# Kernel tuning notes

Measured on AMD Instinct MI355X. Metric: run time of the kernel, lower is better.

## Reference

```python
import jax, jax.numpy as jnp
import numpy as np

B, C, H, W = 4, 512, 48, 48
DQ = C // 8  # inter_rate = 8
N = H * W
EPS = 1e-5


def _local_mask(radius):
    r = np.arange(N) // W
    c = np.arange(N) % W
    d = np.maximum(np.abs(r[:, None] - r[None, :]), np.abs(c[:, None] - c[None, :]))
    return jnp.asarray(d <= radius)


def setup_inputs() -> dict:
    key = jax.random.key(0)
    ks = jax.random.split(key, 12)
    def nrm(k, shape, scale=0.04):
        return jax.random.normal(k, shape, dtype=jnp.float32) * scale
    zc = jnp.zeros((C,), jnp.float32)
    oc = jnp.ones((C,), jnp.float32)
    return {
        "x": jax.random.normal(ks[0], (B, C, H, W), dtype=jnp.float32),
        "Wq": nrm(ks[1], (DQ, C)), "bq": jnp.zeros((DQ,), jnp.float32),
        "Wk": nrm(ks[2], (DQ, C)), "bk": jnp.zeros((DQ,), jnp.float32),
        "Wv": nrm(ks[3], (C, C)), "bv": zc,
        "conv1_w": nrm(ks[4], (C, C, 3, 3)),
        "bn1_w": oc, "bn1_b": zc, "bn1_m": zc, "bn1_v": oc,
        "conv2_w": nrm(ks[5], (C, C, 3, 3)),
        "bn2_w": oc, "bn2_b": zc, "bn2_m": zc, "bn2_v": oc,
        "sig1_w": nrm(ks[6], (C, C)), "sig1_b": zc,
        "sig2_w": nrm(ks[7], (C, C)), "sig2_b": zc,
        "gamma": jnp.full((1,), 0.5, jnp.float32),
        "gamma1": jnp.full((1,), 0.3, jnp.float32),
        "gamma2": jnp.full((1,), 0.2, jnp.float32),
        "mask1": _local_mask(6),
        "mask2": _local_mask(12),
    }


def _masked_softmax(e, mask):
    # exp(e)*mask / sum(exp(e)*mask) == softmax with -inf outside mask
    e = e - jnp.max(e, axis=-1, keepdims=True)
    w = jnp.exp(e) * mask.astype(e.dtype)
    return w / jnp.sum(w, axis=-1, keepdims=True)


def _conv1x1(t, w, b):
    return jnp.einsum('bchw,dc->bdhw', t, w) + b[None, :, None, None]


def _conv3x3_bn_relu(t, w, g, beta, mu, var):
    y = jax.lax.conv_general_dilated(t, w, (1, 1), 'SAME',
                                     dimension_numbers=('NCHW', 'OIHW', 'NCHW'))
    scale = (g / jnp.sqrt(var + EPS))[None, :, None, None]
    y = (y - mu[None, :, None, None]) * scale + beta[None, :, None, None]
    return jax.nn.relu(y)


def _forward(x, Wq, bq, Wk, bk, Wv, bv, conv1_w, bn1_w, bn1_b, bn1_m, bn1_v,
             conv2_w, bn2_w, bn2_b, bn2_m, bn2_v, sig1_w, sig1_b, sig2_w, sig2_b,
             gamma, gamma1, gamma2, mask1, mask2):
    b, c, h, w = x.shape
    n = h * w
    q = _conv1x1(x, Wq, bq).reshape(b, -1, n)   # [B, d, N]
    k = _conv1x1(x, Wk, bk).reshape(b, -1, n)   # [B, d, N]
    energy = jnp.einsum('bdn,bdm->bnm', q, k)   # [B, N, N] (query rows)
    a0 = jax.nn.softmax(energy, axis=-1)
    a1 = _masked_softmax(energy, mask1)
    a2 = _masked_softmax(energy, mask2)
    v = _conv1x1(x, Wv, bv).reshape(b, c, n)
    # torch: bmm(value, attention.permute(0,2,1)) -> out[b,c,m] = sum_n v[b,c,n]*a[m,n]
    out0 = jnp.einsum('bcn,bmn->bcm', v, a0).reshape(b, c, h, w)
    out0 = gamma * out0 + x
    out0 = _conv3x3_bn_relu(out0, conv1_w, bn1_w, bn1_b, bn1_m, bn1_v)
    s1 = (jax.nn.sigmoid(_conv1x1(out0, sig1_w, sig1_b)) * out0).reshape(b, c, n)
    out1 = jnp.einsum('bcn,bmn->bcm', s1, a1).reshape(b, c, h, w)
    out1 = gamma1 * out1 + out0
    out1 = _conv3x3_bn_relu(out1, conv2_w, bn2_w, bn2_b, bn2_m, bn2_v)
    s2 = (jax.nn.sigmoid(_conv1x1(out1, sig2_w, sig2_b)) * out1).reshape(b, c, n)
    out2 = jnp.einsum('bcn,bmn->bcm', s2, a2).reshape(b, c, h, w)
    return gamma2 * out2 + out1


def reference(x, Wq, bq, Wk, bk, Wv, bv, conv1_w, bn1_w, bn1_b, bn1_m, bn1_v,
              conv2_w, bn2_w, bn2_b, bn2_m, bn2_v, sig1_w, sig1_b, sig2_w, sig2_b,
              gamma, gamma1, gamma2, mask1, mask2):
    return _forward(x, Wq, bq, Wk, bk, Wv, bv, conv1_w, bn1_w, bn1_b, bn1_m, bn1_v,
                    conv2_w, bn2_w, bn2_b, bn2_m, bn2_v, sig1_w, sig1_b, sig2_w, sig2_b,
                    gamma, gamma1, gamma2, mask1, mask2)
```

## Files before the change

### kernel.cpp

```cpp
#include <hip/hip_runtime.h>
#include <math.h>

#define BB 4
#define CC 512
#define HH 48
#define WW 48
#define NN 2304
#define DDQ 64
#define LDSP 72
#define PW 50
#define PROWS 2500

typedef __attribute__((ext_vector_type(4))) float f32x4;
typedef __attribute__((ext_vector_type(8))) _Float16 half8;
typedef __attribute__((ext_vector_type(4))) _Float16 half4;
typedef __attribute__((ext_vector_type(8))) short bf16x8;

__device__ __forceinline__ int imax(int a, int b) { return a > b ? a : b; }
__device__ __forceinline__ int imin(int a, int b) { return a < b ? a : b; }
__device__ __forceinline__ int prow(int m) {
    int h = m / WW, w = m - h * WW;
    return (h + 1) * PW + (w + 1);
}
__device__ __forceinline__ unsigned short f2bf(float f) {
    unsigned u = __float_as_uint(f);
    u += 0x7fffu + ((u >> 16) & 1u);
    return (unsigned short)(u >> 16);
}
__device__ __forceinline__ float bf2f(unsigned short s) {
    unsigned u = ((unsigned)s) << 16;
    return __uint_as_float(u);
}

typedef __attribute__((address_space(1))) unsigned int g_u32;
typedef __attribute__((address_space(3))) unsigned int l_u32;
__device__ __forceinline__ void gl16(const void* g, void* l) {
    __builtin_amdgcn_global_load_lds((const g_u32*)g, (l_u32*)l, 16, 0, 0);
}

#define WAIT6()  asm volatile("s_waitcnt vmcnt(6)" ::: "memory")
#define WAIT0()  asm volatile("s_waitcnt vmcnt(0)" ::: "memory")
#define BAR()    { __builtin_amdgcn_s_barrier(); asm volatile("" ::: "memory"); }

#define BWAVE_IDX()                                  \
    int tid = threadIdx.x;                           \
    int wave = tid >> 6, lane = tid & 63;            \
    int wm = (wave >> 1) * 64, wn = (wave & 1) * 32; \
    int x = lane & 15, qq = lane >> 4;

__device__ __forceinline__ half8 fragld(const _Float16* T, int r, int c) {
    int kb = c ^ (r & 7);
    return *(const half8*)(T + r * 64 + kb * 8);
}
__device__ __forceinline__ bf16x8 fragld_b(const unsigned short* T, int r, int c) {
    int kb = c ^ (r & 7);
    return *(const bf16x8*)(T + r * 64 + kb * 8);
}

__device__ __forceinline__ void btile(const _Float16* As, const _Float16* Bs,
                                      f32x4 acc[4][2], int wm, int wn, int x, int qq) {
#pragma unroll
    for (int ks = 0; ks < 2; ++ks) {
        int c = ks * 4 + qq;
        half8 a0 = fragld(As, wm + x, c);
        half8 a1 = fragld(As, wm + 16 + x, c);
        half8 a2 = fragld(As, wm + 32 + x, c);
        half8 a3 = fragld(As, wm + 48 + x, c);
        half8 b0 = fragld(Bs, wn + x, c);
        half8 b1 = fragld(Bs, wn + 16 + x, c);
        acc[0][0] = __builtin_amdgcn_mfma_f32_16x16x32_f16(a0, b0, acc[0][0], 0, 0, 0);
        acc[0][1] = __builtin_amdgcn_mfma_f32_16x16x32_f16(a0, b1, acc[0][1], 0, 0, 0);
        acc[1][0] = __builtin_amdgcn_mfma_f32_16x16x32_f16(a1, b0, acc[1][0], 0, 0, 0);
        acc[1][1] = __builtin_amdgcn_mfma_f32_16x16x32_f16(a1, b1, acc[1][1], 0, 0, 0);
        acc[2][0] = __builtin_amdgcn_mfma_f32_16x16x32_f16(a2, b0, acc[2][0], 0, 0, 0);
        acc[2][1] = __builtin_amdgcn_mfma_f32_16x16x32_f16(a2, b1, acc[2][1], 0, 0, 0);
        acc[3][0] = __builtin_amdgcn_mfma_f32_16x16x32_f16(a3, b0, acc[3][0], 0, 0, 0);
        acc[3][1] = __builtin_amdgcn_mfma_f32_16x16x32_f16(a3, b1, acc[3][1], 0, 0, 0);
    }
}
__device__ __forceinline__ void btile_b(const unsigned short* As, const unsigned short* Bs,
                                        f32x4 acc[4][2], int wm, int wn, int x, int qq) {
#pragma unroll
    for (int ks = 0; ks < 2; ++ks) {
        int c = ks * 4 + qq;
        bf16x8 a0 = fragld_b(As, wm + x, c);
        bf16x8 a1 = fragld_b(As, wm + 16 + x, c);
        bf16x8 a2 = fragld_b(As, wm + 32 + x, c);
        bf16x8 a3 = fragld_b(As, wm + 48 + x, c);
        bf16x8 b0 = fragld_b(Bs, wn + x, c);
        bf16x8 b1 = fragld_b(Bs, wn + 16 + x, c);
        acc[0][0] = __builtin_amdgcn_mfma_f32_16x16x32_bf16(a0, b0, acc[0][0], 0, 0, 0);
        acc[0][1] = __builtin_amdgcn_mfma_f32_16x16x32_bf16(a0, b1, acc[0][1], 0, 0, 0);
        acc[1][0] = __builtin_amdgcn_mfma_f32_16x16x32_bf16(a1, b0, acc[1][0], 0, 0, 0);
        acc[1][1] = __builtin_amdgcn_mfma_f32_16x16x32_bf16(a1, b1, acc[1][1], 0, 0, 0);
        acc[2][0] = __builtin_amdgcn_mfma_f32_16x16x32_bf16(a2, b0, acc[2][0], 0, 0, 0);
        acc[2][1] = __builtin_amdgcn_mfma_f32_16x16x32_bf16(a2, b1, acc[2][1], 0, 0, 0);
        acc[3][0] = __builtin_amdgcn_mfma_f32_16x16x32_bf16(a3, b0, acc[3][0], 0, 0, 0);
        acc[3][1] = __builtin_amdgcn_mfma_f32_16x16x32_bf16(a3, b1, acc[3][1], 0, 0, 0);
    }
}

#define BACC_INIT()                                         \
    f32x4 zf = {0.f, 0.f, 0.f, 0.f};                        \
    f32x4 acc[4][2];                                        \
    _Pragma("unroll") for (int i_ = 0; i_ < 4; ++i_) {      \
        acc[i_][0] = zf; acc[i_][1] = zf; }

#define SLOT_A(i) int sb = (wave * 4 + (i)) * 64; int s = sb + lane; \
                  int r = s >> 3, kb = s & 7; int koff = ((kb ^ (r & 7)) << 3);
#define SLOT_B(i) int sb = (wave * 2 + (i)) * 64; int s = sb + lane; \
                  int r = s >> 3, kb = s & 7; int koff = ((kb ^ (r & 7)) << 3);

__device__ __forceinline__ void stage_rows(_Float16* dst, const _Float16* __restrict__ src,
                                           int ld, int row0, int k0, int tid) {
#pragma unroll
    for (int i = 0; i < 2; ++i) {
        int s = tid * 2 + i;
        int r = s >> 3, off = (s & 7) << 3;
        *(half8*)(dst + r * LDSP + off) =
            *(const half8*)(src + (size_t)(row0 + r) * ld + k0 + off);
    }
}
__device__ __forceinline__ void mfma_tile(const _Float16* As, const _Float16* Bs,
                                          f32x4 acc[2][2], int wm, int wn, int x, int qq) {
#pragma unroll
    for (int ks = 0; ks < 2; ++ks) {
        int kof = ks * 32 + qq * 8;
        half8 a0 = *(const half8*)(As + (wm + x) * LDSP + kof);
        half8 a1 = *(const half8*)(As + (wm + 16 + x) * LDSP + kof);
        half8 b0 = *(const half8*)(Bs + (wn + x) * LDSP + kof);
        half8 b1 = *(const half8*)(Bs + (wn + 16 + x) * LDSP + kof);
        acc[0][0] = __builtin_amdgcn_mfma_f32_16x16x32_f16(a0, b0, acc[0][0], 0, 0, 0);
        acc[0][1] = __builtin_amdgcn_mfma_f32_16x16x32_f16(a0, b1, acc[0][1], 0, 0, 0);
        acc[1][0] = __builtin_amdgcn_mfma_f32_16x16x32_f16(a1, b0, acc[1][0], 0, 0, 0);
        acc[1][1] = __builtin_amdgcn_mfma_f32_16x16x32_f16(a1, b1, acc[1][1], 0, 0, 0);
    }
}
#define WAVE_IDX()                             \
    int tid = threadIdx.x;                     \
    int wave = tid >> 6, lane = tid & 63;      \
    int wm = (wave >> 1) * 32, wn = (wave & 1) * 32; \
    int x = lane & 15, qq = lane >> 4;
#define ACC_INIT()                             \
    f32x4 zf = {0.f, 0.f, 0.f, 0.f};           \
    f32x4 acc[2][2];                           \
    acc[0][0] = zf; acc[0][1] = zf; acc[1][0] = zf; acc[1][1] = zf;

__global__ __launch_bounds__(256) void k_cast_multi(const float* __restrict__ s0,
                                                    const float* __restrict__ s1,
                                                    const float* __restrict__ s2,
                                                    _Float16* __restrict__ d0,
                                                    _Float16* __restrict__ d1,
                                                    _Float16* __restrict__ d2, int n) {
    const float* s = blockIdx.y == 0 ? s0 : (blockIdx.y == 1 ? s1 : s2);
    _Float16* d = blockIdx.y == 0 ? d0 : (blockIdx.y == 1 ? d1 : d2);
    for (int i = blockIdx.x * 256 + threadIdx.x; i < n; i += gridDim.x * 256)
        d[i] = (_Float16)s[i];
}

__global__ __launch_bounds__(256) void k_repack_conv2(const float* __restrict__ w1,
                                                      const float* __restrict__ w2,
                                                      _Float16* __restrict__ d1,
                                                      _Float16* __restrict__ d2) {
    const float* w = blockIdx.y ? w2 : w1;
    _Float16* dst = blockIdx.y ? d2 : d1;
    int i = blockIdx.x * 256 + threadIdx.x;
    if (i >= 9 * CC * CC) return;
    int r = i / (CC * CC);
    int rem = i - r * CC * CC;
    int co = rem / CC, ci = rem - (rem / CC) * CC;
    dst[i] = (_Float16)w[((size_t)co * CC + ci) * 9 + r];
}

__global__ __launch_bounds__(256) void k_transpose_x(const float* __restrict__ x,
                                                     _Float16* __restrict__ xT) {
    __shared__ float tile[32][33];
    int b = blockIdx.z;
    int c0 = blockIdx.y * 32, n0 = blockIdx.x * 32;
    int tx = threadIdx.x & 31, ty = threadIdx.x >> 5;
    const float* xb = x + (size_t)b * CC * NN;
#pragma unroll
    for (int rr = 0; rr < 32; rr += 8)
        tile[ty + rr][tx] = xb[(size_t)(c0 + ty + rr) * NN + n0 + tx];
    __syncthreads();
    _Float16* xTb = xT + (size_t)b * NN * CC;
#pragma unroll
    for (int rr = 0; rr < 32; rr += 8)
        xTb[(size_t)(n0 + ty + rr) * CC + c0 + tx] = (_Float16)tile[tx][ty + rr];
}

__global__ __launch_bounds__(256) void k_qkproj(const _Float16* __restrict__ Wq,
                                                const _Float16* __restrict__ Wk,
                                                const float* __restrict__ bq,
                                                const float* __restrict__ bk,
                                                const _Float16* __restrict__ xT,
                                                _Float16* __restrict__ qT,
                                                _Float16* __restrict__ kT) {
    __shared__ _Float16 As[64 * LDSP];
    __shared__ _Float16 Bs[64 * LDSP];
    WAVE_IDX();
    int j0 = blockIdx.x * 64, b = blockIdx.z;
    const _Float16* Wp = blockIdx.y ? Wk : Wq;
    const float* bias = blockIdx.y ? bk : bq;
    _Float16* outT = blockIdx.y ? kT : qT;
    const _Float16* xTb = xT + (size_t)b * NN * CC;
    ACC_INIT();
    for (int kc = 0; kc < CC; kc += 64) {
        stage_rows(As, Wp, CC, 0, kc, tid);
        stage_rows(Bs, xTb, CC, j0, kc, tid);
        __syncthreads();
        mfma_tile(As, Bs, acc, wm, wn, x, qq);
        __syncthreads();
    }
#pragma unroll
    for (int ms = 0; ms < 2; ++ms) {
        int R0 = wm + ms * 16 + qq * 4;
#pragma unroll
        for (int ns = 0; ns < 2; ++ns) {
            int Ccol = j0 + wn + ns * 16 + x;
            half4 t;
            t.x = (_Float16)(acc[ms][ns][0] + bias[R0 + 0]);
            t.y = (_Float16)(acc[ms][ns][1] + bias[R0 + 1]);
            t.z = (_Float16)(acc[ms][ns][2] + bias[R0 + 2]);
            t.w = (_Float16)(acc[ms][ns][3] + bias[R0 + 3]);
            *(half4*)(outT + ((size_t)b * NN + Ccol) * DDQ + R0) = t;
        }
    }
}

template <int EPI, int PAD>
__global__ __launch_bounds__(256) void k_cgemm(const _Float16* __restrict__ W,
                                               const float* __restrict__ bias,
                                               const _Float16* __restrict__ Bsrc,
                                               const float* __restrict__ gate,
                                               unsigned short* __restrict__ out) {
    __shared__ __align__(16) _Float16 As[2][128 * 64];
    __shared__ __align__(16) _Float16 Bs[2][64 * 64];
    BWAVE_IDX();
    int j0 = blockIdx.x * 64, i0 = blockIdx.y * 128, b = blockIdx.z;
    const _Float16* Bb = Bsrc + (size_t)b * (PAD ? (size_t)PROWS * CC : (size_t)NN * CC);

    const _Float16* aSrc[4]; int aOf[4];
#pragma unroll
    for (int i = 0; i < 4; ++i) {
        SLOT_A(i);
        aSrc[i] = W + (size_t)(i0 + r) * CC + koff;
        aOf[i] = sb * 8;
    }
    const _Float16* bSrc[2]; int bOf[2];
#pragma unroll
    for (int i = 0; i < 2; ++i) {
        SLOT_B(i);
        int row = PAD ? prow(j0 + r) : (j0 + r);
        bSrc[i] = Bb + (size_t)row * CC + koff;
        bOf[i] = sb * 8;
    }
    BACC_INIT();
#define STG_G(kc, nb)                                                          \
    { _Pragma("unroll") for (int i = 0; i < 4; ++i)                            \
          gl16(aSrc[i] + (kc), As[nb] + aOf[i]);                               \
      _Pragma("unroll") for (int i = 0; i < 2; ++i)                            \
          gl16(bSrc[i] + (kc), Bs[nb] + bOf[i]); }
    STG_G(0, 0);
    STG_G(64, 1);
    const int NSTEP = CC / 64;
#pragma unroll
    for (int t = 0; t + 2 < NSTEP; ++t) {
        WAIT6();
        BAR();
        btile(As[t & 1], Bs[t & 1], acc, wm, wn, x, qq);
        BAR();
        STG_G((t + 2) * 64, (t & 1));
    }
    WAIT6();
    BAR();
    btile(As[(NSTEP - 2) & 1], Bs[(NSTEP - 2) & 1], acc, wm, wn, x, qq);
    WAIT0();
    BAR();
    btile(As[(NSTEP - 1) & 1], Bs[(NSTEP - 1) & 1], acc, wm, wn, x, qq);
#undef STG_G
#pragma unroll
    for (int mt = 0; mt < 4; ++mt) {
        int R0 = i0 + wm + mt * 16 + qq * 4;
#pragma unroll
        for (int nt = 0; nt < 2; ++nt) {
            int Ccol = j0 + wn + nt * 16 + x;
#pragma unroll
            for (int e = 0; e < 4; ++e) {
                float v = acc[mt][nt][e] + bias[R0 + e];
                size_t idx = ((size_t)b * CC + R0 + e) * NN + Ccol;
                if (EPI == 1) v = gate[idx] / (1.f + __expf(-v));
                out[idx] = f2bf(v);
            }
        }
    }
}

__global__ __launch_bounds__(256) void k_exp(const _Float16* __restrict__ qT,
                                             const _Float16* __restrict__ kT,
                                             unsigned short* __restrict__ attnB,
                                             float* __restrict__ rowsum, int rad) {
    __shared__ _Float16 qs[64 * LDSP];
    __shared__ _Float16 ks[64 * LDSP];
    __shared__ unsigned short Eh[64 * 72];
    __shared__ float psum[512];
    WAVE_IDX();
    int j0 = blockIdx.x * 64, i0 = blockIdx.y * 64, b = blockIdx.z;
    if (rad > 0) {
        int hlo = i0 / WW, hhi = (i0 + 63) / WW;
        int h2lo = imax(0, hlo - rad), h2hi = imin(HH - 1, hhi + rad);
        int klo = (h2lo * WW) & ~63;
        int khi = imin(NN, ((h2hi + 1) * WW + 63) & ~63);
        if (j0 + 64 <= klo || j0 >= khi) return;
    }
    stage_rows(qs, qT + (size_t)b * NN * DDQ, DDQ, i0, 0, tid);
    stage_rows(ks, kT + (size_t)b * NN * DDQ, DDQ, j0, 0, tid);
    __syncthreads();
    ACC_INIT();
    mfma_tile(qs, ks, acc, wm, wn, x, qq);
#pragma unroll
    for (int ns = 0; ns < 2; ++ns) {
        int col = wn + ns * 16 + x;
        int gn = j0 + col;
        int hn = gn / WW, cn = gn % WW;
#pragma unroll
        for (int ms = 0; ms < 2; ++ms)
#pragma unroll
            for (int e = 0; e < 4; ++e) {
                int row = wm + ms * 16 + qq * 4 + e;
                int gm = i0 + row;
                bool valid = true;
                if (rad > 0) {
                    int dh = gm / WW - hn; if (dh < 0) dh = -dh;
                    int dc = gm % WW - cn; if (dc < 0) dc = -dc;
                    valid = (dh <= rad) && (dc <= rad);
                }
                float w = valid ? __expf(acc[ms][ns][e]) : 0.f;
                Eh[row * 72 + col] = f2bf(w);
            }
    }
    __syncthreads();
#pragma unroll
    for (int t = 0; t < 2; ++t) {
        int s = tid + t * 256;
        int r = s >> 3, cg = (s & 7) << 3;
        bf16x8 v = *(const bf16x8*)(Eh + r * 72 + cg);
        *(bf16x8*)(attnB + ((size_t)b * NN + i0 + r) * NN + j0 + cg) = v;
        float ss = 0.f;
#pragma unroll
        for (int j = 0; j < 8; ++j) ss += bf2f((unsigned short)v[j]);
        psum[s] = ss;
    }
    __syncthreads();
    if (tid < 64) {
        float tot = 0.f;
#pragma unroll
        for (int g = 0; g < 8; ++g) tot += psum[tid * 8 + g];
        atomicAdd(rowsum + (size_t)b * NN + i0 + tid, tot);
    }
}

__global__ __launch_bounds__(256) void k_attn(const unsigned short* __restrict__ A,
                                              const unsigned short* __restrict__ attnB,
                                              const float* __restrict__ rowsum,
                                              const float* __restrict__ res,
                                              const float* __restrict__ gamma,
                                              float* __restrict__ outF,
                                              _Float16* __restrict__ outT, int rad) {
    __shared__ __align__(16) unsigned short As[2][128 * 64];
    __shared__ __align__(16) unsigned short Bs[2][64 * 64];
    BWAVE_IDX();
    int j0 = blockIdx.x * 64, i0 = blockIdx.y * 128, b = blockIdx.z;
    int klo = 0, khi = NN;
    if (rad > 0) {
        int hlo = j0 / WW, hhi = (j0 + 63) / WW;
        int h2lo = imax(0, hlo - rad), h2hi = imin(HH - 1, hhi + rad);
        klo = (h2lo * WW) & ~63;
        khi = imin(NN, ((h2hi + 1) * WW + 63) & ~63);
    }
    const unsigned short* Ab = A + (size_t)b * CC * NN;
    const unsigned short* Tb = attnB + (size_t)b * NN * NN;

    const unsigned short* aSrc[4]; int aOf[4];
#pragma unroll
    for (int i = 0; i < 4; ++i) {
        SLOT_A(i);
        aSrc[i] = Ab + (size_t)(i0 + r) * NN + koff + klo;
        aOf[i] = sb * 8;
    }
    const unsigned short* bSrc[2]; int bOf[2];
#pragma unroll
    for (int i = 0; i < 2; ++i) {
        SLOT_B(i);
        bSrc[i] = Tb + (size_t)(j0 + r) * NN + koff + klo;
        bOf[i] = sb * 8;
    }
    BACC_INIT();
    int nsteps = (khi - klo) >> 6;
#define STG_T(kc, nb)                                                          \
    { _Pragma("unroll") for (int i = 0; i < 4; ++i)                            \
          gl16(aSrc[i] + (kc), As[nb] + aOf[i]);                               \
      _Pragma("unroll") for (int i = 0; i < 2; ++i)                            \
          gl16(bSrc[i] + (kc), Bs[nb] + bOf[i]); }
    STG_T(0, 0);
    STG_T(64, 1);
    for (int t = 0; t + 2 < nsteps; ++t) {
        WAIT6();
        BAR();
        btile_b(As[t & 1], Bs[t & 1], acc, wm, wn, x, qq);
        BAR();
        STG_T((t + 2) << 6, (t & 1));
    }
    WAIT6();
    BAR();
    btile_b(As[(nsteps - 2) & 1], Bs[(nsteps - 2) & 1], acc, wm, wn, x, qq);
    WAIT0();
    BAR();
    btile_b(As[(nsteps - 1) & 1], Bs[(nsteps - 1) & 1], acc, wm, wn, x, qq);
#undef STG_T
    float g = gamma[0];
#pragma unroll
    for (int mt = 0; mt < 4; ++mt) {
        int R0 = i0 + wm + mt * 16 + qq * 4;
#pragma unroll
        for (int nt = 0; nt < 2; ++nt) {
            int Ccol = j0 + wn + nt * 16 + x;
            float linv = g / fmaxf(rowsum[(size_t)b * NN + Ccol], 1e-30f);
            float v[4];
#pragma unroll
            for (int e = 0; e < 4; ++e)
                v[e] = acc[mt][nt][e] * linv + res[((size_t)b * CC + R0 + e) * NN + Ccol];
            if (outT) {
                half4 t;
                t.x = (_Float16)v[0]; t.y = (_Float16)v[1];
                t.z = (_Float16)v[2]; t.w = (_Float16)v[3];
                *(half4*)(outT + ((size_t)b * PROWS + prow(Ccol)) * CC + R0) = t;
            }
            if (outF) {
#pragma unroll
                for (int e = 0; e < 4; ++e)
                    outF[((size_t)b * CC + R0 + e) * NN + Ccol] = v[e];
            }
        }
    }
}

__global__ __launch_bounds__(256) void k_conv3(const _Float16* __restrict__ Arep,
                                               const _Float16* __restrict__ Tpad,
                                               const float* __restrict__ bng,
                                               const float* __restrict__ bnb,
                                               const float* __restrict__ bnm,
                                               const float* __restrict__ bnv,
                                               float* __restrict__ outF,
                                               _Float16* __restrict__ outT) {
    __shared__ __align__(16) _Float16 As[2][128 * 64];
    __shared__ __align__(16) _Float16 Bs[2][64 * 64];
    BWAVE_IDX();
    int j0 = blockIdx.x * 64, i0 = blockIdx.y * 128, b = blockIdx.z;
    const _Float16* Tb = Tpad + (size_t)b * PROWS * CC;

    const _Float16* aBase[4]; int aOf[4];
#pragma unroll
    for (int i = 0; i < 4; ++i) {
        SLOT_A(i);
        aBase[i] = Arep + (size_t)(i0 + r) * CC + koff;
        aOf[i] = sb * 8;
    }
    const _Float16* bBase[2]; int bOf[2];
#pragma unroll
    for (int i = 0; i < 2; ++i) {
        SLOT_B(i);
        bBase[i] = Tb + (size_t)prow(j0 + r) * CC + koff;
        bOf[i] = sb * 8;
    }
    BACC_INIT();

#define STAGE_CONV(u, nb)                                                       \
    {                                                                           \
        int rt_ = (u) >> 3, ci_ = ((u) & 7) << 6;                               \
        int r3_ = rt_ / 3;                                                      \
        ptrdiff_t aoff_ = (ptrdiff_t)rt_ * (CC * CC) + ci_;                     \
        ptrdiff_t boff_ =                                                       \
            (ptrdiff_t)((r3_ - 1) * PW + (rt_ - r3_ * 3 - 1)) * CC + ci_;       \
        _Pragma("unroll") for (int i = 0; i < 4; ++i)                           \
            gl16(aBase[i] + aoff_, As[nb] + aOf[i]);                            \
        _Pragma("unroll") for (int i = 0; i < 2; ++i)                           \
            gl16(bBase[i] + boff_, Bs[nb] + bOf[i]);                            \
    }

    STAGE_CONV(0, 0);
    STAGE_CONV(1, 1);
    const int TOT = 9 * (CC / 64);
#pragma unroll 2
    for (int t = 0; t + 2 < TOT; ++t) {
        WAIT6();
        BAR();
        btile(As[t & 1], Bs[t & 1], acc, wm, wn, x, qq);
        BAR();
        STAGE_CONV(t + 2, (t & 1));
    }
    WAIT6();
    BAR();
    btile(As[(TOT - 2) & 1], Bs[(TOT - 2) & 1], acc, wm, wn, x, qq);
    WAIT0();
    BAR();
    btile(As[(TOT - 1) & 1], Bs[(TOT - 1) & 1], acc, wm, wn, x, qq);
#undef STAGE_CONV

#pragma unroll
    for (int mt = 0; mt < 4; ++mt) {
        int R0 = i0 + wm + mt * 16 + qq * 4;
        float sc[4], sh[4];
#pragma unroll
        for (int e = 0; e < 4; ++e) {
            sc[e] = bng[R0 + e] * rsqrtf(bnv[R0 + e] + 1e-5f);
            sh[e] = bnb[R0 + e] - bnm[R0 + e] * sc[e];
        }
#pragma unroll
        for (int nt = 0; nt < 2; ++nt) {
            int Ccol = j0 + wn + nt * 16 + x;
            float v[4];
#pragma unroll
            for (int e = 0; e < 4; ++e) {
                float t = acc[mt][nt][e] * sc[e] + sh[e];
                v[e] = t > 0.f ? t : 0.f;
                outF[((size_t)b * CC + R0 + e) * NN + Ccol] = v[e];
            }
            half4 t4;
            t4.x = (_Float16)v[0]; t4.y = (_Float16)v[1];
            t4.z = (_Float16)v[2]; t4.w = (_Float16)v[3];
            *(half4*)(outT + ((size_t)b * PROWS + prow(Ccol)) * CC + R0) = t4;
        }
    }
}

extern "C" void kernel_launch(void* const* d_in, const int* in_sizes, int n_in,
                              void* d_out, int out_size, void* d_ws, size_t ws_size,
                              hipStream_t stream) {
    const float* xin  = (const float*)d_in[0];
    const float* Wq   = (const float*)d_in[1];
    const float* bq   = (const float*)d_in[2];
    const float* Wk   = (const float*)d_in[3];
    const float* bk   = (const float*)d_in[4];
    const float* Wv   = (const float*)d_in[5];
    const float* bv   = (const float*)d_in[6];
    const float* c1w  = (const float*)d_in[7];
    const float* bn1w = (const float*)d_in[8];
    const float* bn1b = (const float*)d_in[9];
    const float* bn1m = (const float*)d_in[10];
    const float* bn1v = (const float*)d_in[11];
    const float* c2w  = (const float*)d_in[12];
    const float* bn2w = (const float*)d_in[13];
    const float* bn2b = (const float*)d_in[14];
    const float* bn2m = (const float*)d_in[15];
    const float* bn2v = (const float*)d_in[16];
    const float* s1w  = (const float*)d_in[17];
    const float* s1b  = (const float*)d_in[18];
    const float* s2w  = (const float*)d_in[19];
    const float* s2b  = (const float*)d_in[20];
    const float* gamma  = (const float*)d_in[21];
    const float* gamma1 = (const float*)d_in[22];
    const float* gamma2 = (const float*)d_in[23];

    float* out = (float*)d_out;

    char* p = (char*)d_ws;
    unsigned short* attn = (unsigned short*)p; p += (size_t)BB * NN * NN * 2;
    _Float16* xT    = (_Float16*)p; p += (size_t)BB * NN * CC * 2;
    _Float16* qT    = (_Float16*)p; p += (size_t)BB * NN * DDQ * 2;
    _Float16* kT    = (_Float16*)p; p += (size_t)BB * NN * DDQ * 2;
    unsigned short* vsB = (unsigned short*)p; p += (size_t)BB * CC * NN * 2;
    _Float16* TattnP= (_Float16*)p; p += (size_t)BB * PROWS * CC * 2;
    _Float16* TconvP= (_Float16*)p; p += (size_t)BB * PROWS * CC * 2;
    float*    rR    = (float*)p;    p += (size_t)BB * CC * NN * 4;
    _Float16* wq_h  = (_Float16*)p; p += (size_t)DDQ * CC * 2;
    _Float16* wk_h  = (_Float16*)p; p += (size_t)DDQ * CC * 2;
    _Float16* wv_h  = (_Float16*)p; p += (size_t)CC * CC * 2;
    _Float16* s1_h  = (_Float16*)p; p += (size_t)CC * CC * 2;
    _Float16* s2_h  = (_Float16*)p; p += (size_t)CC * CC * 2;
    _Float16* crep1 = (_Float16*)p; p += (size_t)9 * CC * CC * 2;
    _Float16* crep2 = (_Float16*)p; p += (size_t)9 * CC * CC * 2;
    float*    rowsum= (float*)p;    p += (size_t)3 * BB * NN * 4;

    dim3 blk(256);

    hipMemsetAsync(TattnP, 0, (size_t)BB * PROWS * CC * 2, stream);
    hipMemsetAsync(TconvP, 0, (size_t)BB * PROWS * CC * 2, stream);
    hipMemsetAsync(rowsum, 0, (size_t)3 * BB * NN * 4, stream);

    k_cast_multi<<<dim3(128, 2), blk, 0, stream>>>(Wq, Wk, nullptr, wq_h, wk_h, nullptr, DDQ * CC);
    k_cast_multi<<<dim3(1024, 3), blk, 0, stream>>>(Wv, s1w, s2w, wv_h, s1_h, s2_h, CC * CC);
    k_repack_conv2<<<dim3((9 * CC * CC + 255) / 256, 2), blk, 0, stream>>>(c1w, c2w, crep1, crep2);
    k_transpose_x<<<dim3(NN / 32, CC / 32, BB), blk, 0, stream>>>(xin, xT);

    dim3 gQK(NN / 64, 2, BB);
    dim3 gExp(NN / 64, NN / 64, BB);
    dim3 gBig(NN / 64, CC / 128, BB);

    float* rs0 = rowsum;
    float* rs1 = rowsum + (size_t)BB * NN;
    float* rs2 = rowsum + (size_t)2 * BB * NN;

    k_qkproj<<<gQK, blk, 0, stream>>>(wq_h, wk_h, bq, bk, xT, qT, kT);
    k_cgemm<0, 0><<<gBig, blk, 0, stream>>>(wv_h, bv, xT, nullptr, vsB);

    k_exp<<<gExp, blk, 0, stream>>>(qT, kT, attn, rs0, -1);
    k_attn<<<gBig, blk, 0, stream>>>(vsB, attn, rs0, xin, gamma, nullptr, TattnP, -1);
    k_conv3<<<gBig, blk, 0, stream>>>(crep1, TattnP, bn1w, bn1b, bn1m, bn1v, rR, TconvP);

    k_cgemm<1, 1><<<gBig, blk, 0, stream>>>(s1_h, s1b, TconvP, rR, vsB);
    k_exp<<<gExp, blk, 0, stream>>>(qT, kT, attn, rs1, 6);
    k_attn<<<gBig, blk, 0, stream>>>(vsB, attn, rs1, rR, gamma1, nullptr, TattnP, 6);
    k_conv3<<<gBig, blk, 0, stream>>>(crep2, TattnP, bn2w, bn2b, bn2m, bn2v, rR, TconvP);

    k_cgemm<1, 1><<<gBig, blk, 0, stream>>>(s2_h, s2b, TconvP, rR, vsB);
    k_exp<<<gExp, blk, 0, stream>>>(qT, kT, attn, rs2, 12);
    k_attn<<<gBig, blk, 0, stream>>>(vsB, attn, rs2, rR, gamma2, out, nullptr, 12);
}
```

Before: 488.3 us.

## Swizzle big-GEMM blocks across XCDs and read residuals from fp16 padded buffer

Flattens the grid of the big GEMM kernels (cgemm, attn, conv3) to 1D and remaps block indices so consecutive tiles of the same batch land on the same XCD, improving L2 reuse. The sigmoid-gate and residual inputs are now read from the fp16 padded transposed conv output (half4 loads) instead of a separate fp32 NCHW buffer. That lets the first conv3 skip its fp32 output write. This cuts global traffic and strided fp32 loads, at the cost of using fp16-rounded residual and gate values.

Result: faster. 452.2 us (median of 3 runs) (-7.4%).

```diff
diff --git a/kernel.cpp b/kernel.cpp
--- a/kernel.cpp
+++ b/kernel.cpp
@@ -41,6 +41,12 @@
 #define WAIT6()  asm volatile("s_waitcnt vmcnt(6)" ::: "memory")
 #define WAIT0()  asm volatile("s_waitcnt vmcnt(0)" ::: "memory")
 #define BAR()    { __builtin_amdgcn_s_barrier(); asm volatile("" ::: "memory"); }
+
+#define BIG_DECODE()                                          \
+    int raw = blockIdx.x;                                     \
+    int wg = ((raw & 7) * 72) + (raw >> 3);                   \
+    int jx = wg % 36; int rem = wg / 36;                      \
+    int j0 = jx * 64, i0 = (rem & 3) * 128, b = rem >> 2;
 
 #define BWAVE_IDX()                                  \
     int tid = threadIdx.x;                           \
@@ -232,12 +238,12 @@
 __global__ __launch_bounds__(256) void k_cgemm(const _Float16* __restrict__ W,
                                                const float* __restrict__ bias,
                                                const _Float16* __restrict__ Bsrc,
-                                               const float* __restrict__ gate,
+                                               const _Float16* __restrict__ gateH,
                                                unsigned short* __restrict__ out) {
     __shared__ __align__(16) _Float16 As[2][128 * 64];
     __shared__ __align__(16) _Float16 Bs[2][64 * 64];
     BWAVE_IDX();
-    int j0 = blockIdx.x * 64, i0 = blockIdx.y * 128, b = blockIdx.z;
+    BIG_DECODE();
     const _Float16* Bb = Bsrc + (size_t)b * (PAD ? (size_t)PROWS * CC : (size_t)NN * CC);
 
     const _Float16* aSrc[4]; int aOf[4];
@@ -285,11 +291,14 @@
 #pragma unroll
         for (int nt = 0; nt < 2; ++nt) {
             int Ccol = j0 + wn + nt * 16 + x;
+            half4 gh;
+            if (EPI == 1)
+                gh = *(const half4*)(gateH + ((size_t)b * PROWS + prow(Ccol)) * CC + R0);
 #pragma unroll
             for (int e = 0; e < 4; ++e) {
                 float v = acc[mt][nt][e] + bias[R0 + e];
                 size_t idx = ((size_t)b * CC + R0 + e) * NN + Ccol;
-                if (EPI == 1) v = gate[idx] / (1.f + __expf(-v));
+                if (EPI == 1) v = (float)gh[e] / (1.f + __expf(-v));
                 out[idx] = f2bf(v);
             }
         }
@@ -363,14 +372,15 @@
 __global__ __launch_bounds__(256) void k_attn(const unsigned short* __restrict__ A,
                                               const unsigned short* __restrict__ attnB,
                                               const float* __restrict__ rowsum,
-                                              const float* __restrict__ res,
+                                              const float* __restrict__ resF,
+                                              const _Float16* __restrict__ resH,
                                               const float* __restrict__ gamma,
                                               float* __restrict__ outF,
                                               _Float16* __restrict__ outT, int rad) {
     __shared__ __align__(16) unsigned short As[2][128 * 64];
     __shared__ __align__(16) unsigned short Bs[2][64 * 64];
     BWAVE_IDX();
-    int j0 = blockIdx.x * 64, i0 = blockIdx.y * 128, b = blockIdx.z;
+    BIG_DECODE();
     int klo = 0, khi = NN;
     if (rad > 0) {
         int hlo = j0 / WW, hhi = (j0 + 63) / WW;
@@ -427,9 +437,16 @@
             int Ccol = j0 + wn + nt * 16 + x;
             float linv = g / fmaxf(rowsum[(size_t)b * NN + Ccol], 1e-30f);
             float v[4];
-#pragma unroll
-            for (int e = 0; e < 4; ++e)
-                v[e] = acc[mt][nt][e] * linv + res[((size_t)b * CC + R0 + e) * NN + Ccol];
+            if (resH) {
+                half4 rh = *(const half4*)(resH + ((size_t)b * PROWS + prow(Ccol)) * CC + R0);
+#pragma unroll
+                for (int e = 0; e < 4; ++e)
+                    v[e] = acc[mt][nt][e] * linv + (float)rh[e];
+            } else {
+#pragma unroll
+                for (int e = 0; e < 4; ++e)
+                    v[e] = acc[mt][nt][e] * linv + resF[((size_t)b * CC + R0 + e) * NN + Ccol];
+            }
             if (outT) {
                 half4 t;
                 t.x = (_Float16)v[0]; t.y = (_Float16)v[1];
@@ -456,7 +473,7 @@
     __shared__ __align__(16) _Float16 As[2][128 * 64];
     __shared__ __align__(16) _Float16 Bs[2][64 * 64];
     BWAVE_IDX();
-    int j0 = blockIdx.x * 64, i0 = blockIdx.y * 128, b = blockIdx.z;
+    BIG_DECODE();
     const _Float16* Tb = Tpad + (size_t)b * PROWS * CC;
 
     const _Float16* aBase[4]; int aOf[4];
@@ -524,7 +541,11 @@
             for (int e = 0; e < 4; ++e) {
                 float t = acc[mt][nt][e] * sc[e] + sh[e];
                 v[e] = t > 0.f ? t : 0.f;
-                outF[((size_t)b * CC + R0 + e) * NN + Ccol] = v[e];
+            }
+            if (outF) {
+#pragma unroll
+                for (int e = 0; e < 4; ++e)
+                    outF[((size_t)b * CC + R0 + e) * NN + Ccol] = v[e];
             }
             half4 t4;
             t4.x = (_Float16)v[0]; t4.y = (_Float16)v[1];
@@ -595,7 +616,7 @@
 
     dim3 gQK(NN / 64, 2, BB);
     dim3 gExp(NN / 64, NN / 64, BB);
-    dim3 gBig(NN / 64, CC / 128, BB);
+    dim3 gBig(576);
 
     float* rs0 = rowsum;
     float* rs1 = rowsum + (size_t)BB * NN;
@@ -605,15 +626,15 @@
     k_cgemm<0, 0><<<gBig, blk, 0, stream>>>(wv_h, bv, xT, nullptr, vsB);
 
     k_exp<<<gExp, blk, 0, stream>>>(qT, kT, attn, rs0, -1);
-    k_attn<<<gBig, blk, 0, stream>>>(vsB, attn, rs0, xin, gamma, nullptr, TattnP, -1);
-    k_conv3<<<gBig, blk, 0, stream>>>(crep1, TattnP, bn1w, bn1b, bn1m, bn1v, rR, TconvP);
-
-    k_cgemm<1, 1><<<gBig, blk, 0, stream>>>(s1_h, s1b, TconvP, rR, vsB);
+    k_attn<<<gBig, blk, 0, stream>>>(vsB, attn, rs0, xin, nullptr, gamma, nullptr, TattnP, -1);
+    k_conv3<<<gBig, blk, 0, stream>>>(crep1, TattnP, bn1w, bn1b, bn1m, bn1v, nullptr, TconvP);
+
+    k_cgemm<1, 1><<<gBig, blk, 0, stream>>>(s1_h, s1b, TconvP, TconvP, vsB);
     k_exp<<<gExp, blk, 0, stream>>>(qT, kT, attn, rs1, 6);
-    k_attn<<<gBig, blk, 0, stream>>>(vsB, attn, rs1, rR, gamma1, nullptr, TattnP, 6);
+    k_attn<<<gBig, blk, 0, stream>>>(vsB, attn, rs1, nullptr, TconvP, gamma1, nullptr, TattnP, 6);
     k_conv3<<<gBig, blk, 0, stream>>>(crep2, TattnP, bn2w, bn2b, bn2m, bn2v, rR, TconvP);
 
-    k_cgemm<1, 1><<<gBig, blk, 0, stream>>>(s2_h, s2b, TconvP, rR, vsB);
+    k_cgemm<1, 1><<<gBig, blk, 0, stream>>>(s2_h, s2b, TconvP, TconvP, vsB);
     k_exp<<<gExp, blk, 0, stream>>>(qT, kT, attn, rs2, 12);
-    k_attn<<<gBig, blk, 0, stream>>>(vsB, attn, rs2, rR, gamma2, out, nullptr, 12);
-}
+    k_attn<<<gBig, blk, 0, stream>>>(vsB, attn, rs2, rR, nullptr, gamma2, out, nullptr, 12);
+}
```
